# Kernel tuning notes

Measured on AMD Instinct MI355X. Metric: run time of the kernel, lower is better.

The kernel has to match this reference:

```python
import jax, jax.numpy as jnp
import numpy as np

N, K, D, H = 10000, 30, 128, 4
DH = D // H
E = N * K

def setup_inputs() -> dict:
    ks = jax.random.split(jax.random.key(0), 12)
    s = 0.05
    h = jax.random.normal(ks[0], (N, D), jnp.float32)
    e = jax.random.normal(ks[1], (E, D), jnp.float32)
    # edges grouped by source node, K neighbors each (required by the (i j) rearranges)
    src = jnp.repeat(jnp.arange(N, dtype=jnp.int32), K)
    dst = jax.random.randint(ks[2], (E,), 0, N, dtype=jnp.int32)
    edge_index = jnp.stack([src, dst], axis=0)
    return {
        'h': h, 'e': e, 'edge_index': edge_index,
        'att_w1': jax.random.normal(ks[3], (3 * D, D)) * s, 'att_b1': jnp.zeros((D,)),
        'att_w2': jax.random.normal(ks[4], (D, D)) * s,     'att_b2': jnp.zeros((D,)),
        'att_w3': jax.random.normal(ks[5], (D, H)) * s,     'att_b3': jnp.zeros((H,)),
        'node_w1': jax.random.normal(ks[6], (2 * D, D)) * s, 'node_b1': jnp.zeros((D,)),
        'node_w2': jax.random.normal(ks[7], (D, D)) * s,     'node_b2': jnp.zeros((D,)),
        'node_w3': jax.random.normal(ks[8], (D, D)) * s,     'node_b3': jnp.zeros((D,)),
        'to_h_w': jax.random.normal(ks[9], (D, D)) * s,
    }

def reference(h, e, edge_index, att_w1, att_b1, att_w2, att_b2, att_w3, att_b3,
              node_w1, node_b1, node_w2, node_b2, node_w3, node_b3, to_h_w):
    gelu = lambda x: jax.nn.gelu(x, approximate=False)  # torch nn.GELU default (erf)
    hi = h[edge_index[0]]                               # [E, D] gather
    hj = h[edge_index[1]]                               # [E, D] gather
    hi_eij_hj = jnp.concatenate([hi, e, hj], axis=-1)   # [E, 3D]
    eij_hj = jnp.concatenate([e, hj], axis=-1)          # [E, 2D]
    # attention logits per head
    w = jax.nn.relu(hi_eij_hj @ att_w1 + att_b1)
    w = jax.nn.relu(w @ att_w2 + att_b2)
    w = (w @ att_w3 + att_b3).reshape(N, K, H)          # (i j) h -> i j h
    w = w / jnp.sqrt(jnp.float32(DH))
    att = jax.nn.softmax(w, axis=1)                     # softmax over neighbors j
    # values per edge, split per head
    v = gelu(eij_hj @ node_w1 + node_b1)
    v = gelu(v @ node_w2 + node_b2)
    v = (v @ node_w3 + node_b3).reshape(N, K, H, DH)    # (i j) (h d) -> i j h d
    out = jnp.einsum('nkh,nkhd->nhd', att, v).reshape(N, D)  # weighted aggregation
    return out @ to_h_w
```

## Files before the change

kernel.cpp:

```cpp
#include <hip/hip_runtime.h>
#include <hip/hip_bf16.h>

#define N_NODES 10000
#define KNEI    30
#define DIM     128
#define EDGES   (N_NODES * KNEI)

typedef __attribute__((ext_vector_type(4))) float  f32x4;
typedef __attribute__((ext_vector_type(8))) __bf16 bf16x8;
typedef __attribute__((ext_vector_type(4))) __bf16 bf16x4;

#define OFF_AW1 0
#define OFF_AW2 49152
#define OFF_NW1 65536
#define OFF_NW2 98304
#define OFF_NW3 114688
#define OFF_TH  131072
#define TOT_TILES 288
#define YHI_BYTE_OFF (300 * 1024)

__global__ __launch_bounds__(256) void repack_all(
    const float* __restrict__ aw1, const float* __restrict__ aw2,
    const float* __restrict__ nw1, const float* __restrict__ nw2,
    const float* __restrict__ nw3, const float* __restrict__ thw,
    __bf16* __restrict__ dst) {
    int t = blockIdx.x * 256 + threadIdx.x;
    if (t >= TOT_TILES * 512) return;
    int tile = t >> 9;
    const float* src; int lt;
    if      (tile < 96)  { src = aw1; lt = tile; }
    else if (tile < 128) { src = aw2; lt = tile - 96; }
    else if (tile < 192) { src = nw1; lt = tile - 128; }
    else if (tile < 224) { src = nw2; lt = tile - 192; }
    else if (tile < 256) { src = nw3; lt = tile - 224; }
    else                 { src = thw; lt = tile - 256; }
    int i    = t & 7;
    int lane = (t >> 3) & 63;
    int nt = lt & 7;
    int kt = lt >> 3;
    int k = kt * 32 + ((lane >> 4) << 3) + i;
    int n = nt * 16 + (lane & 15);
    dst[t] = (__bf16)src[k * DIM + n];
}

__device__ __forceinline__ float gelu_f(float x) {
    float u = 0.7978845608f * (x + 0.044715f * x * x * x);
    float t = 1.f - 2.f / (__expf(2.f * u) + 1.f);
    return 0.5f * x * (1.f + t);
}

__device__ __forceinline__ bf16x4 cvt4(float4 v) {
    bf16x4 r;
    r[0] = (__bf16)v.x; r[1] = (__bf16)v.y; r[2] = (__bf16)v.z; r[3] = (__bf16)v.w;
    return r;
}

__device__ __forceinline__ void mm_lds4(f32x4 acc[2][2], const __bf16* __restrict__ wfrag,
                                        const __bf16* x, int sx, int nkt,
                                        int wv, int lane) {
    const int mrow = lane & 15;
    const int kgrp = lane >> 4;
#pragma unroll
    for (int kt = 0; kt < nkt; ++kt) {
        bf16x8 a0 = *reinterpret_cast<const bf16x8*>(wfrag + ((kt * 8 + wv * 2 + 0) * 64 + lane) * 8);
        bf16x8 a1 = *reinterpret_cast<const bf16x8*>(wfrag + ((kt * 8 + wv * 2 + 1) * 64 + lane) * 8);
        const int kb = kt * 32 + kgrp * 8;
        bf16x8 b0 = *reinterpret_cast<const bf16x8*>(x + mrow * sx + kb);
        bf16x8 b1 = *reinterpret_cast<const bf16x8*>(x + (16 + mrow) * sx + kb);
        acc[0][0] = __builtin_amdgcn_mfma_f32_16x16x32_bf16(a0, b0, acc[0][0], 0, 0, 0);
        acc[0][1] = __builtin_amdgcn_mfma_f32_16x16x32_bf16(a0, b1, acc[0][1], 0, 0, 0);
        acc[1][0] = __builtin_amdgcn_mfma_f32_16x16x32_bf16(a1, b0, acc[1][0], 0, 0, 0);
        acc[1][1] = __builtin_amdgcn_mfma_f32_16x16x32_bf16(a1, b1, acc[1][1], 0, 0, 0);
    }
}

__device__ __forceinline__ void store_act4(f32x4 acc[2][2], const float* __restrict__ bias,
                                           __bf16* y, int sy, int actmode,
                                           int wv, int lane) {
    const int mrow = lane & 15;
    const int kgrp = lane >> 4;
#pragma unroll
    for (int nt = 0; nt < 2; ++nt) {
        const int nb = wv * 32 + nt * 16 + kgrp * 4;
        float b0 = bias[nb], b1 = bias[nb + 1], b2 = bias[nb + 2], b3 = bias[nb + 3];
#pragma unroll
        for (int mf = 0; mf < 2; ++mf) {
            bf16x4 pk;
            float vv[4] = {acc[nt][mf][0] + b0, acc[nt][mf][1] + b1,
                           acc[nt][mf][2] + b2, acc[nt][mf][3] + b3};
#pragma unroll
            for (int r = 0; r < 4; ++r) {
                float v = vv[r];
                v = actmode == 0 ? fmaxf(v, 0.f) : gelu_f(v);
                pk[r] = (__bf16)v;
            }
            *reinterpret_cast<bf16x4*>(y + (mf * 16 + mrow) * sy + nb) = pk;
        }
    }
}

#define ZERO4(A) do { A[0][0]=(f32x4){0.f,0.f,0.f,0.f}; A[0][1]=(f32x4){0.f,0.f,0.f,0.f}; \
                      A[1][0]=(f32x4){0.f,0.f,0.f,0.f}; A[1][1]=(f32x4){0.f,0.f,0.f,0.f}; } while (0)

__global__ __launch_bounds__(512) void mm128(const float* __restrict__ in,
                                             float* __restrict__ outp,
                                             const __bf16* __restrict__ wfrag,
                                             const float* __restrict__ bias) {
    __shared__ __bf16 sP[64 * 136];
    const int tid  = threadIdx.x;
    const int wv   = tid >> 6;
    const int lane = tid & 63;
    const int mrow = lane & 15;
    const int kgrp = lane >> 4;
    const int base = blockIdx.x * 64;

#pragma unroll
    for (int c = 0; c < 4; ++c) {
        int idx = c * 512 + tid;
        int m  = idx >> 5;
        int jv = idx & 31;
        int row = base + m;
        float4 v = make_float4(0.f, 0.f, 0.f, 0.f);
        if (row < N_NODES) v = *reinterpret_cast<const float4*>(in + (long)row * DIM + jv * 4);
        *reinterpret_cast<bf16x4*>(&sP[m * 136 + jv * 4]) = cvt4(v);
    }
    __syncthreads();

    f32x4 acc[4];
#pragma unroll
    for (int mf = 0; mf < 4; ++mf) acc[mf] = (f32x4){0.f, 0.f, 0.f, 0.f};
#pragma unroll
    for (int kt = 0; kt < 4; ++kt) {
        bf16x8 a = *reinterpret_cast<const bf16x8*>(wfrag + ((kt * 8 + wv) * 64 + lane) * 8);
        const int kb = kt * 32 + kgrp * 8;
#pragma unroll
        for (int mf = 0; mf < 4; ++mf) {
            bf16x8 b = *reinterpret_cast<const bf16x8*>(sP + (mf * 16 + mrow) * 136 + kb);
            acc[mf] = __builtin_amdgcn_mfma_f32_16x16x32_bf16(a, b, acc[mf], 0, 0, 0);
        }
    }
    const int nb = wv * 16 + kgrp * 4;
    float b0 = 0.f, b1 = 0.f, b2 = 0.f, b3 = 0.f;
    if (bias) { b0 = bias[nb]; b1 = bias[nb + 1]; b2 = bias[nb + 2]; b3 = bias[nb + 3]; }
#pragma unroll
    for (int mf = 0; mf < 4; ++mf) {
        int row = base + mf * 16 + mrow;
        if (row < N_NODES) {
            float4 o = make_float4(acc[mf][0] + b0, acc[mf][1] + b1,
                                   acc[mf][2] + b2, acc[mf][3] + b3);
            *reinterpret_cast<float4*>(outp + (long)row * DIM + nb) = o;
        }
    }
}

__global__ __launch_bounds__(256, 4) void gnn_fused(
    const float* __restrict__ h, const float* __restrict__ e, const int* __restrict__ eidx,
    const float* __restrict__ yhi,
    const float* __restrict__ ab2, const float* __restrict__ aw3, const float* __restrict__ ab3,
    const float* __restrict__ nb1, const float* __restrict__ nb2, const float* __restrict__ nb3,
    const __bf16* __restrict__ wp, float* __restrict__ pre_out) {

    __shared__ __bf16 S[32 * 264];
    __shared__ __bf16 Y1[32 * 136];
    __shared__ __bf16 Y2[32 * 136];
    __shared__ float  sLogW[4][32][4];
    __shared__ float  sW[32][4];

    const int tid  = threadIdx.x;
    const int wv   = tid >> 6;
    const int lane = tid & 63;
    const int mrow = lane & 15;
    const int kg   = lane >> 4;
    const int node = blockIdx.x;
    const long ebase = (long)node * KNEI;

#pragma unroll
    for (int c = 0; c < 4; ++c) {
        int idx = c * 256 + tid;
        int m  = idx >> 5;
        int jv = idx & 31;
        float4 ev = make_float4(0.f, 0.f, 0.f, 0.f), hjv = ev;
        if (m < KNEI) {
            long ge = ebase + m;
            ev  = *reinterpret_cast<const float4*>(e + ge * DIM + jv * 4);
            int dstn = eidx[EDGES + ge];
            hjv = *reinterpret_cast<const float4*>(h + (long)dstn * DIM + jv * 4);
        }
        *reinterpret_cast<bf16x4*>(&S[m * 264 + jv * 4])       = cvt4(ev);
        *reinterpret_cast<bf16x4*>(&S[m * 264 + 128 + jv * 4]) = cvt4(hjv);
    }
    __syncthreads();

    f32x4 acc[2][2];

    ZERO4(acc);
    mm_lds4(acc, wp + OFF_AW1 + 16384, S, 264, 8, wv, lane);
    store_act4(acc, yhi + (long)node * DIM, Y1, 136, 0, wv, lane);
    __syncthreads();

    {
        ZERO4(acc);
        mm_lds4(acc, wp + OFF_AW2, Y1, 136, 4, wv, lane);
        float lp[2][4];
        lp[0][0]=lp[0][1]=lp[0][2]=lp[0][3]=0.f;
        lp[1][0]=lp[1][1]=lp[1][2]=lp[1][3]=0.f;
#pragma unroll
        for (int nt = 0; nt < 2; ++nt) {
            const int nb = wv * 32 + nt * 16 + kg * 4;
            float b0 = ab2[nb], b1 = ab2[nb + 1], b2 = ab2[nb + 2], b3 = ab2[nb + 3];
            float4 w3v[4];
#pragma unroll
            for (int r = 0; r < 4; ++r)
                w3v[r] = *reinterpret_cast<const float4*>(aw3 + (nb + r) * 4);
#pragma unroll
            for (int mf = 0; mf < 2; ++mf) {
                float vv[4] = {acc[nt][mf][0] + b0, acc[nt][mf][1] + b1,
                               acc[nt][mf][2] + b2, acc[nt][mf][3] + b3};
#pragma unroll
                for (int r = 0; r < 4; ++r) {
                    float v = fmaxf(vv[r], 0.f);
                    lp[mf][0] += v * w3v[r].x;
                    lp[mf][1] += v * w3v[r].y;
                    lp[mf][2] += v * w3v[r].z;
                    lp[mf][3] += v * w3v[r].w;
                }
            }
        }
#pragma unroll
        for (int mf = 0; mf < 2; ++mf)
#pragma unroll
            for (int hh = 0; hh < 4; ++hh) {
                lp[mf][hh] += __shfl_xor(lp[mf][hh], 16);
                lp[mf][hh] += __shfl_xor(lp[mf][hh], 32);
            }
        if (kg == 0) {
#pragma unroll
            for (int mf = 0; mf < 2; ++mf) {
                float4 o = make_float4(lp[mf][0], lp[mf][1], lp[mf][2], lp[mf][3]);
                *reinterpret_cast<float4*>(&sLogW[wv][mf * 16 + mrow][0]) = o;
            }
        }
    }
    ZERO4(acc);
    mm_lds4(acc, wp + OFF_NW1, S, 264, 8, wv, lane);
    store_act4(acc, nb1, Y2, 136, 1, wv, lane);
    __syncthreads();

    if (tid < 128) {
        int m = tid >> 2, hh = tid & 3;
        float s = ab3[hh];
#pragma unroll
        for (int w = 0; w < 4; ++w) s += sLogW[w][m][hh];
        sLogW[0][m][hh] = s * 0.17677669529f;
    }
    ZERO4(acc);
    mm_lds4(acc, wp + OFF_NW2, Y2, 136, 4, wv, lane);
    store_act4(acc, nb2, Y1, 136, 1, wv, lane);
    __syncthreads();

    if (wv == 0 && lane < 32) {
        float4 lg = (lane < KNEI) ? *reinterpret_cast<float4*>(&sLogW[0][lane][0])
                                  : make_float4(-1e30f, -1e30f, -1e30f, -1e30f);
        float4 mx = lg;
#pragma unroll
        for (int msk = 1; msk <= 16; msk <<= 1) {
            mx.x = fmaxf(mx.x, __shfl_xor(mx.x, msk));
            mx.y = fmaxf(mx.y, __shfl_xor(mx.y, msk));
            mx.z = fmaxf(mx.z, __shfl_xor(mx.z, msk));
            mx.w = fmaxf(mx.w, __shfl_xor(mx.w, msk));
        }
        float4 ex = make_float4(__expf(lg.x - mx.x), __expf(lg.y - mx.y),
                                __expf(lg.z - mx.z), __expf(lg.w - mx.w));
        float4 sm = ex;
#pragma unroll
        for (int msk = 1; msk <= 16; msk <<= 1) {
            sm.x += __shfl_xor(sm.x, msk);
            sm.y += __shfl_xor(sm.y, msk);
            sm.z += __shfl_xor(sm.z, msk);
            sm.w += __shfl_xor(sm.w, msk);
        }
        float4 w = make_float4(ex.x / sm.x, ex.y / sm.y, ex.z / sm.z, ex.w / sm.w);
        *reinterpret_cast<float4*>(&sW[lane][0]) = w;
    }
    ZERO4(acc);
    mm_lds4(acc, wp + OFF_NW3, Y1, 136, 4, wv, lane);
    __syncthreads();

    {
        float wgt0 = sW[mrow][wv];
        float wgt1 = sW[16 + mrow][wv];
        float part[2][4];
#pragma unroll
        for (int nt = 0; nt < 2; ++nt)
#pragma unroll
            for (int r = 0; r < 4; ++r)
                part[nt][r] = wgt0 * acc[nt][0][r] + wgt1 * acc[nt][1][r];
#pragma unroll
        for (int msk = 1; msk <= 8; msk <<= 1)
#pragma unroll
            for (int nt = 0; nt < 2; ++nt)
#pragma unroll
                for (int r = 0; r < 4; ++r)
                    part[nt][r] += __shfl_xor(part[nt][r], msk);
        if (mrow == 0) {
#pragma unroll
            for (int nt = 0; nt < 2; ++nt) {
                const int nb = wv * 32 + nt * 16 + kg * 4;
                float4 o = make_float4(part[nt][0] + nb3[nb],     part[nt][1] + nb3[nb + 1],
                                       part[nt][2] + nb3[nb + 2], part[nt][3] + nb3[nb + 3]);
                *reinterpret_cast<float4*>(pre_out + (long)node * DIM + nb) = o;
            }
        }
    }
}

extern "C" void kernel_launch(void* const* d_in, const int* in_sizes, int n_in,
                              void* d_out, int out_size, void* d_ws, size_t ws_size,
                              hipStream_t stream) {
    const float* h   = (const float*)d_in[0];
    const float* e   = (const float*)d_in[1];
    const int*   ei  = (const int*)d_in[2];
    const float* aw1 = (const float*)d_in[3];
    const float* ab1 = (const float*)d_in[4];
    const float* aw2 = (const float*)d_in[5];
    const float* ab2 = (const float*)d_in[6];
    const float* aw3 = (const float*)d_in[7];
    const float* ab3 = (const float*)d_in[8];
    const float* nw1 = (const float*)d_in[9];
    const float* nb1 = (const float*)d_in[10];
    const float* nw2 = (const float*)d_in[11];
    const float* nb2 = (const float*)d_in[12];
    const float* nw3 = (const float*)d_in[13];
    const float* nb3 = (const float*)d_in[14];
    const float* thw = (const float*)d_in[15];
    float* out = (float*)d_out;
    __bf16* wp = (__bf16*)d_ws;
    float* yhi = (float*)((char*)d_ws + YHI_BYTE_OFF);

    repack_all<<<TOT_TILES * 2, 256, 0, stream>>>(aw1, aw2, nw1, nw2, nw3, thw, wp);

    const int nblk = (N_NODES + 63) / 64;
    mm128<<<nblk, 512, 0, stream>>>(h, yhi, wp + OFF_AW1, ab1);

    gnn_fused<<<N_NODES, 256, 0, stream>>>(h, e, ei, yhi, ab2, aw3, ab3,
                                           nb1, nb2, nb3, wp, out);
    mm128<<<nblk, 512, 0, stream>>>(out, out, wp + OFF_TH, nullptr);
}
```

Before: 179.7 us.

## Merge attention and value MLP layers into wide concatenated GEMMs with shared LDS

Repacks weights so the first layers of the attention and value MLPs form one 256-wide GEMM over the shared [e,hj] tile, and the second layers form one block-diagonal-style pass where waves 0-1 handle attention and waves 2-3 handle values. This reuses each B fragment across four MFMAs and cuts the number of separate matmul phases and barriers. LDS is collapsed into one reused buffer and the occupancy hint is raised from 4 to 6 blocks. The cost is more accumulator registers per wave (acc[4][2]) and uneven epilogue work between attention and value waves.

```diff
diff --git a/kernel.cpp b/kernel.cpp
--- a/kernel.cpp
+++ b/kernel.cpp
@@ -10,11 +10,10 @@
 typedef __attribute__((ext_vector_type(8))) __bf16 bf16x8;
 typedef __attribute__((ext_vector_type(4))) __bf16 bf16x4;
 
-#define OFF_AW1 0
-#define OFF_AW2 49152
-#define OFF_NW1 65536
-#define OFF_NW2 98304
-#define OFF_NW3 114688
+#define OFF_CW1 0
+#define OFF_CW2 65536
+#define OFF_NW3 98304
+#define OFF_HI  114688
 #define OFF_TH  131072
 #define TOT_TILES 288
 #define YHI_BYTE_OFF (300 * 1024)
@@ -27,20 +26,28 @@
     int t = blockIdx.x * 256 + threadIdx.x;
     if (t >= TOT_TILES * 512) return;
     int tile = t >> 9;
-    const float* src; int lt;
-    if      (tile < 96)  { src = aw1; lt = tile; }
-    else if (tile < 128) { src = aw2; lt = tile - 96; }
-    else if (tile < 192) { src = nw1; lt = tile - 128; }
-    else if (tile < 224) { src = nw2; lt = tile - 192; }
-    else if (tile < 256) { src = nw3; lt = tile - 224; }
-    else                 { src = thw; lt = tile - 256; }
     int i    = t & 7;
     int lane = (t >> 3) & 63;
-    int nt = lt & 7;
-    int kt = lt >> 3;
-    int k = kt * 32 + ((lane >> 4) << 3) + i;
-    int n = nt * 16 + (lane & 15);
-    dst[t] = (__bf16)src[k * DIM + n];
+    int krow = ((lane >> 4) << 3) + i;
+    int ncol = lane & 15;
+    float v;
+    if (tile < 128) {
+        int kt = tile >> 4, nt = tile & 15;
+        int k = kt * 32 + krow, n = nt * 16 + ncol;
+        v = (n < 128) ? aw1[(128 + k) * 128 + n] : nw1[k * 128 + (n - 128)];
+    } else if (tile < 192) {
+        int lt = tile - 128;
+        int kt = lt >> 4, nt = lt & 15;
+        int k = kt * 32 + krow, n = nt * 16 + ncol;
+        v = (n < 128) ? aw2[k * 128 + n] : nw2[k * 128 + (n - 128)];
+    } else {
+        int lt = tile & 31;
+        int kt = lt >> 3, nt = lt & 7;
+        int k = kt * 32 + krow, n = nt * 16 + ncol;
+        const float* s = (tile < 224) ? nw3 : (tile < 256) ? aw1 : thw;
+        v = s[k * 128 + n];
+    }
+    dst[t] = (__bf16)v;
 }
 
 __device__ __forceinline__ float gelu_f(float x) {
@@ -54,53 +61,6 @@
     r[0] = (__bf16)v.x; r[1] = (__bf16)v.y; r[2] = (__bf16)v.z; r[3] = (__bf16)v.w;
     return r;
 }
-
-__device__ __forceinline__ void mm_lds4(f32x4 acc[2][2], const __bf16* __restrict__ wfrag,
-                                        const __bf16* x, int sx, int nkt,
-                                        int wv, int lane) {
-    const int mrow = lane & 15;
-    const int kgrp = lane >> 4;
-#pragma unroll
-    for (int kt = 0; kt < nkt; ++kt) {
-        bf16x8 a0 = *reinterpret_cast<const bf16x8*>(wfrag + ((kt * 8 + wv * 2 + 0) * 64 + lane) * 8);
-        bf16x8 a1 = *reinterpret_cast<const bf16x8*>(wfrag + ((kt * 8 + wv * 2 + 1) * 64 + lane) * 8);
-        const int kb = kt * 32 + kgrp * 8;
-        bf16x8 b0 = *reinterpret_cast<const bf16x8*>(x + mrow * sx + kb);
-        bf16x8 b1 = *reinterpret_cast<const bf16x8*>(x + (16 + mrow) * sx + kb);
-        acc[0][0] = __builtin_amdgcn_mfma_f32_16x16x32_bf16(a0, b0, acc[0][0], 0, 0, 0);
-        acc[0][1] = __builtin_amdgcn_mfma_f32_16x16x32_bf16(a0, b1, acc[0][1], 0, 0, 0);
-        acc[1][0] = __builtin_amdgcn_mfma_f32_16x16x32_bf16(a1, b0, acc[1][0], 0, 0, 0);
-        acc[1][1] = __builtin_amdgcn_mfma_f32_16x16x32_bf16(a1, b1, acc[1][1], 0, 0, 0);
-    }
-}
-
-__device__ __forceinline__ void store_act4(f32x4 acc[2][2], const float* __restrict__ bias,
-                                           __bf16* y, int sy, int actmode,
-                                           int wv, int lane) {
-    const int mrow = lane & 15;
-    const int kgrp = lane >> 4;
-#pragma unroll
-    for (int nt = 0; nt < 2; ++nt) {
-        const int nb = wv * 32 + nt * 16 + kgrp * 4;
-        float b0 = bias[nb], b1 = bias[nb + 1], b2 = bias[nb + 2], b3 = bias[nb + 3];
-#pragma unroll
-        for (int mf = 0; mf < 2; ++mf) {
-            bf16x4 pk;
-            float vv[4] = {acc[nt][mf][0] + b0, acc[nt][mf][1] + b1,
-                           acc[nt][mf][2] + b2, acc[nt][mf][3] + b3};
-#pragma unroll
-            for (int r = 0; r < 4; ++r) {
-                float v = vv[r];
-                v = actmode == 0 ? fmaxf(v, 0.f) : gelu_f(v);
-                pk[r] = (__bf16)v;
-            }
-            *reinterpret_cast<bf16x4*>(y + (mf * 16 + mrow) * sy + nb) = pk;
-        }
-    }
-}
-
-#define ZERO4(A) do { A[0][0]=(f32x4){0.f,0.f,0.f,0.f}; A[0][1]=(f32x4){0.f,0.f,0.f,0.f}; \
-                      A[1][0]=(f32x4){0.f,0.f,0.f,0.f}; A[1][1]=(f32x4){0.f,0.f,0.f,0.f}; } while (0)
 
 __global__ __launch_bounds__(512) void mm128(const float* __restrict__ in,
                                              float* __restrict__ outp,
@@ -153,17 +113,15 @@
     }
 }
 
-__global__ __launch_bounds__(256, 4) void gnn_fused(
+__global__ __launch_bounds__(256, 6) void gnn_fused(
     const float* __restrict__ h, const float* __restrict__ e, const int* __restrict__ eidx,
     const float* __restrict__ yhi,
     const float* __restrict__ ab2, const float* __restrict__ aw3, const float* __restrict__ ab3,
     const float* __restrict__ nb1, const float* __restrict__ nb2, const float* __restrict__ nb3,
     const __bf16* __restrict__ wp, float* __restrict__ pre_out) {
 
-    __shared__ __bf16 S[32 * 264];
-    __shared__ __bf16 Y1[32 * 136];
-    __shared__ __bf16 Y2[32 * 136];
-    __shared__ float  sLogW[4][32][4];
+    __shared__ __bf16 U[8704];
+    __shared__ float  sLP[2][32][4];
     __shared__ float  sW[32][4];
 
     const int tid  = threadIdx.x;
@@ -186,36 +144,95 @@
             int dstn = eidx[EDGES + ge];
             hjv = *reinterpret_cast<const float4*>(h + (long)dstn * DIM + jv * 4);
         }
-        *reinterpret_cast<bf16x4*>(&S[m * 264 + jv * 4])       = cvt4(ev);
-        *reinterpret_cast<bf16x4*>(&S[m * 264 + 128 + jv * 4]) = cvt4(hjv);
-    }
-    __syncthreads();
-
-    f32x4 acc[2][2];
-
-    ZERO4(acc);
-    mm_lds4(acc, wp + OFF_AW1 + 16384, S, 264, 8, wv, lane);
-    store_act4(acc, yhi + (long)node * DIM, Y1, 136, 0, wv, lane);
-    __syncthreads();
-
-    {
-        ZERO4(acc);
-        mm_lds4(acc, wp + OFF_AW2, Y1, 136, 4, wv, lane);
+        *reinterpret_cast<bf16x4*>(&U[m * 264 + jv * 4])       = cvt4(ev);
+        *reinterpret_cast<bf16x4*>(&U[m * 264 + 128 + jv * 4]) = cvt4(hjv);
+    }
+    __syncthreads();
+
+    f32x4 acc[4][2];
+#pragma unroll
+    for (int j = 0; j < 4; ++j) { acc[j][0] = (f32x4){0.f,0.f,0.f,0.f}; acc[j][1] = (f32x4){0.f,0.f,0.f,0.f}; }
+
+    {
+        const __bf16* b0p = U + mrow * 264;
+        const __bf16* b1p = U + (16 + mrow) * 264;
+#pragma unroll
+        for (int kt = 0; kt < 8; ++kt) {
+            const int kb = kt * 32 + kg * 8;
+            bf16x8 b0 = *reinterpret_cast<const bf16x8*>(b0p + kb);
+            bf16x8 b1 = *reinterpret_cast<const bf16x8*>(b1p + kb);
+#pragma unroll
+            for (int j = 0; j < 4; ++j) {
+                bf16x8 a = *reinterpret_cast<const bf16x8*>(wp + OFF_CW1 + (size_t)((kt * 16 + wv * 4 + j) * 64 + lane) * 8);
+                acc[j][0] = __builtin_amdgcn_mfma_f32_16x16x32_bf16(a, b0, acc[j][0], 0, 0, 0);
+                acc[j][1] = __builtin_amdgcn_mfma_f32_16x16x32_bf16(a, b1, acc[j][1], 0, 0, 0);
+            }
+        }
+    }
+    __syncthreads();
+
+    {
+        const bool isatt = (wv < 2);
+        __bf16* Y = U + (isatt ? 0 : 4352);
+        const float* yrow = yhi + (long)node * DIM;
+#pragma unroll
+        for (int j = 0; j < 4; ++j) {
+            const int f = (wv & 1) * 64 + j * 16 + kg * 4;
+            float b0, b1, b2, b3;
+            if (isatt) { b0 = yrow[f]; b1 = yrow[f+1]; b2 = yrow[f+2]; b3 = yrow[f+3]; }
+            else       { b0 = nb1[f];  b1 = nb1[f+1];  b2 = nb1[f+2];  b3 = nb1[f+3]; }
+#pragma unroll
+            for (int mf = 0; mf < 2; ++mf) {
+                float vv[4] = {acc[j][mf][0] + b0, acc[j][mf][1] + b1,
+                               acc[j][mf][2] + b2, acc[j][mf][3] + b3};
+                bf16x4 pk;
+#pragma unroll
+                for (int r = 0; r < 4; ++r) {
+                    float v = isatt ? fmaxf(vv[r], 0.f) : gelu_f(vv[r]);
+                    pk[r] = (__bf16)v;
+                }
+                *reinterpret_cast<bf16x4*>(Y + (mf * 16 + mrow) * 136 + f) = pk;
+            }
+        }
+    }
+    __syncthreads();
+
+#pragma unroll
+    for (int j = 0; j < 4; ++j) { acc[j][0] = (f32x4){0.f,0.f,0.f,0.f}; acc[j][1] = (f32x4){0.f,0.f,0.f,0.f}; }
+    {
+        const __bf16* Yb = U + ((wv < 2) ? 0 : 4352);
+        const __bf16* b0p = Yb + mrow * 136;
+        const __bf16* b1p = Yb + (16 + mrow) * 136;
+#pragma unroll
+        for (int kt = 0; kt < 4; ++kt) {
+            const int kb = kt * 32 + kg * 8;
+            bf16x8 b0 = *reinterpret_cast<const bf16x8*>(b0p + kb);
+            bf16x8 b1 = *reinterpret_cast<const bf16x8*>(b1p + kb);
+#pragma unroll
+            for (int j = 0; j < 4; ++j) {
+                bf16x8 a = *reinterpret_cast<const bf16x8*>(wp + OFF_CW2 + (size_t)((kt * 16 + wv * 4 + j) * 64 + lane) * 8);
+                acc[j][0] = __builtin_amdgcn_mfma_f32_16x16x32_bf16(a, b0, acc[j][0], 0, 0, 0);
+                acc[j][1] = __builtin_amdgcn_mfma_f32_16x16x32_bf16(a, b1, acc[j][1], 0, 0, 0);
+            }
+        }
+    }
+
+    if (wv < 2) {
         float lp[2][4];
         lp[0][0]=lp[0][1]=lp[0][2]=lp[0][3]=0.f;
         lp[1][0]=lp[1][1]=lp[1][2]=lp[1][3]=0.f;
 #pragma unroll
-        for (int nt = 0; nt < 2; ++nt) {
-            const int nb = wv * 32 + nt * 16 + kg * 4;
-            float b0 = ab2[nb], b1 = ab2[nb + 1], b2 = ab2[nb + 2], b3 = ab2[nb + 3];
+        for (int j = 0; j < 4; ++j) {
+            const int f = (wv & 1) * 64 + j * 16 + kg * 4;
+            float b0 = ab2[f], b1 = ab2[f+1], b2 = ab2[f+2], b3 = ab2[f+3];
             float4 w3v[4];
 #pragma unroll
             for (int r = 0; r < 4; ++r)
-                w3v[r] = *reinterpret_cast<const float4*>(aw3 + (nb + r) * 4);
+                w3v[r] = *reinterpret_cast<const float4*>(aw3 + (f + r) * 4);
 #pragma unroll
             for (int mf = 0; mf < 2; ++mf) {
-                float vv[4] = {acc[nt][mf][0] + b0, acc[nt][mf][1] + b1,
-                               acc[nt][mf][2] + b2, acc[nt][mf][3] + b3};
+                float vv[4] = {acc[j][mf][0] + b0, acc[j][mf][1] + b1,
+                               acc[j][mf][2] + b2, acc[j][mf][3] + b3};
 #pragma unroll
                 for (int r = 0; r < 4; ++r) {
                     float v = fmaxf(vv[r], 0.f);
@@ -237,30 +254,58 @@
 #pragma unroll
             for (int mf = 0; mf < 2; ++mf) {
                 float4 o = make_float4(lp[mf][0], lp[mf][1], lp[mf][2], lp[mf][3]);
-                *reinterpret_cast<float4*>(&sLogW[wv][mf * 16 + mrow][0]) = o;
-            }
-        }
-    }
-    ZERO4(acc);
-    mm_lds4(acc, wp + OFF_NW1, S, 264, 8, wv, lane);
-    store_act4(acc, nb1, Y2, 136, 1, wv, lane);
-    __syncthreads();
-
-    if (tid < 128) {
-        int m = tid >> 2, hh = tid & 3;
-        float s = ab3[hh];
-#pragma unroll
-        for (int w = 0; w < 4; ++w) s += sLogW[w][m][hh];
-        sLogW[0][m][hh] = s * 0.17677669529f;
-    }
-    ZERO4(acc);
-    mm_lds4(acc, wp + OFF_NW2, Y2, 136, 4, wv, lane);
-    store_act4(acc, nb2, Y1, 136, 1, wv, lane);
-    __syncthreads();
-
+                *reinterpret_cast<float4*>(&sLP[wv][mf * 16 + mrow][0]) = o;
+            }
+        }
+    }
+    __syncthreads();
+
+    if (wv >= 2) {
+#pragma unroll
+        for (int j = 0; j < 4; ++j) {
+            const int f = (wv & 1) * 64 + j * 16 + kg * 4;
+            float b0 = nb2[f], b1 = nb2[f+1], b2 = nb2[f+2], b3 = nb2[f+3];
+#pragma unroll
+            for (int mf = 0; mf < 2; ++mf) {
+                float vv[4] = {acc[j][mf][0] + b0, acc[j][mf][1] + b1,
+                               acc[j][mf][2] + b2, acc[j][mf][3] + b3};
+                bf16x4 pk;
+#pragma unroll
+                for (int r = 0; r < 4; ++r) pk[r] = (__bf16)gelu_f(vv[r]);
+                *reinterpret_cast<bf16x4*>(U + (mf * 16 + mrow) * 136 + f) = pk;
+            }
+        }
+    }
+    __syncthreads();
+
+    f32x4 a2[2][2];
+    a2[0][0]=(f32x4){0.f,0.f,0.f,0.f}; a2[0][1]=(f32x4){0.f,0.f,0.f,0.f};
+    a2[1][0]=(f32x4){0.f,0.f,0.f,0.f}; a2[1][1]=(f32x4){0.f,0.f,0.f,0.f};
+    {
+        const __bf16* b0p = U + mrow * 136;
+        const __bf16* b1p = U + (16 + mrow) * 136;
+#pragma unroll
+        for (int kt = 0; kt < 4; ++kt) {
+            const int kb = kt * 32 + kg * 8;
+            bf16x8 b0 = *reinterpret_cast<const bf16x8*>(b0p + kb);
+            bf16x8 b1 = *reinterpret_cast<const bf16x8*>(b1p + kb);
+#pragma unroll
+            for (int j = 0; j < 2; ++j) {
+                bf16x8 a = *reinterpret_cast<const bf16x8*>(wp + OFF_NW3 + (size_t)((kt * 8 + wv * 2 + j) * 64 + lane) * 8);
+                a2[j][0] = __builtin_amdgcn_mfma_f32_16x16x32_bf16(a, b0, a2[j][0], 0, 0, 0);
+                a2[j][1] = __builtin_amdgcn_mfma_f32_16x16x32_bf16(a, b1, a2[j][1], 0, 0, 0);
+            }
+        }
+    }
     if (wv == 0 && lane < 32) {
-        float4 lg = (lane < KNEI) ? *reinterpret_cast<float4*>(&sLogW[0][lane][0])
-                                  : make_float4(-1e30f, -1e30f, -1e30f, -1e30f);
+        const float s = 0.17677669529f;
+        float4 lg;
+        if (lane < KNEI) {
+            float4 p0 = *reinterpret_cast<float4*>(&sLP[0][lane][0]);
+            float4 p1 = *reinterpret_cast<float4*>(&sLP[1][lane][0]);
+            lg = make_float4((p0.x + p1.x + ab3[0]) * s, (p0.y + p1.y + ab3[1]) * s,
+                             (p0.z + p1.z + ab3[2]) * s, (p0.w + p1.w + ab3[3]) * s);
+        } else lg = make_float4(-1e30f, -1e30f, -1e30f, -1e30f);
         float4 mx = lg;
 #pragma unroll
         for (int msk = 1; msk <= 16; msk <<= 1) {
@@ -282,8 +327,6 @@
         float4 w = make_float4(ex.x / sm.x, ex.y / sm.y, ex.z / sm.z, ex.w / sm.w);
         *reinterpret_cast<float4*>(&sW[lane][0]) = w;
     }
-    ZERO4(acc);
-    mm_lds4(acc, wp + OFF_NW3, Y1, 136, 4, wv, lane);
     __syncthreads();
 
     {
@@ -291,23 +334,23 @@
         float wgt1 = sW[16 + mrow][wv];
         float part[2][4];
 #pragma unroll
-        for (int nt = 0; nt < 2; ++nt)
+        for (int j = 0; j < 2; ++j)
 #pragma unroll
             for (int r = 0; r < 4; ++r)
-                part[nt][r] = wgt0 * acc[nt][0][r] + wgt1 * acc[nt][1][r];
+                part[j][r] = wgt0 * a2[j][0][r] + wgt1 * a2[j][1][r];
 #pragma unroll
         for (int msk = 1; msk <= 8; msk <<= 1)
 #pragma unroll
-            for (int nt = 0; nt < 2; ++nt)
+            for (int j = 0; j < 2; ++j)
 #pragma unroll
                 for (int r = 0; r < 4; ++r)
-                    part[nt][r] += __shfl_xor(part[nt][r], msk);
+                    part[j][r] += __shfl_xor(part[j][r], msk);
         if (mrow == 0) {
 #pragma unroll
-            for (int nt = 0; nt < 2; ++nt) {
-                const int nb = wv * 32 + nt * 16 + kg * 4;
-                float4 o = make_float4(part[nt][0] + nb3[nb],     part[nt][1] + nb3[nb + 1],
-                                       part[nt][2] + nb3[nb + 2], part[nt][3] + nb3[nb + 3]);
+            for (int j = 0; j < 2; ++j) {
+                const int nb = wv * 32 + j * 16 + kg * 4;
+                float4 o = make_float4(part[j][0] + nb3[nb],     part[j][1] + nb3[nb + 1],
+                                       part[j][2] + nb3[nb + 2], part[j][3] + nb3[nb + 3]);
                 *reinterpret_cast<float4*>(pre_out + (long)node * DIM + nb) = o;
             }
         }
@@ -340,7 +383,7 @@
     repack_all<<<TOT_TILES * 2, 256, 0, stream>>>(aw1, aw2, nw1, nw2, nw3, thw, wp);
 
     const int nblk = (N_NODES + 63) / 64;
-    mm128<<<nblk, 512, 0, stream>>>(h, yhi, wp + OFF_AW1, ab1);
+    mm128<<<nblk, 512, 0, stream>>>(h, yhi, wp + OFF_HI, ab1);
 
     gnn_fused<<<N_NODES, 256, 0, stream>>>(h, e, ei, yhi, ab2, aw3, ab3,
                                            nb1, nb2, nb3, wp, out);
```

After: 211.4 us. 17.7% more time.

## Use 8 waves per node block, each owning one 16-column MFMA tile

Applied to the files above, without the earlier changes.

The fused per-node kernel now launches 512 threads (8 waves) instead of 256. Each wave computes a single 16-wide output column tile rather than two, so accumulators shrink from 2x2 to 2 per wave and the logit partial buffer doubles to 8 slots. The NW3 matmul is also moved ahead of the softmax so it can overlap with wave 0's reduction. More waves per block adds latency hiding, but each wave reloads the B fragments from LDS, so LDS traffic doubles and per-CU occupancy may drop under the launch bound.

```diff
diff --git a/kernel.cpp b/kernel.cpp
--- a/kernel.cpp
+++ b/kernel.cpp
@@ -27,6 +27,8 @@
     int t = blockIdx.x * 256 + threadIdx.x;
     if (t >= TOT_TILES * 512) return;
     int tile = t >> 9;
+    int i    = t & 7;
+    int lane = (t >> 3) & 63;
     const float* src; int lt;
     if      (tile < 96)  { src = aw1; lt = tile; }
     else if (tile < 128) { src = aw2; lt = tile - 96; }
@@ -34,8 +36,6 @@
     else if (tile < 224) { src = nw2; lt = tile - 192; }
     else if (tile < 256) { src = nw3; lt = tile - 224; }
     else                 { src = thw; lt = tile - 256; }
-    int i    = t & 7;
-    int lane = (t >> 3) & 63;
     int nt = lt & 7;
     int kt = lt >> 3;
     int k = kt * 32 + ((lane >> 4) << 3) + i;
@@ -55,52 +55,45 @@
     return r;
 }
 
-__device__ __forceinline__ void mm_lds4(f32x4 acc[2][2], const __bf16* __restrict__ wfrag,
-                                        const __bf16* x, int sx, int nkt,
-                                        int wv, int lane) {
+__device__ __forceinline__ void mm_lds(f32x4 acc[2], const __bf16* __restrict__ wfrag,
+                                       const __bf16* x, int sx, int nkt,
+                                       int wv, int lane) {
     const int mrow = lane & 15;
-    const int kgrp = lane >> 4;
+    const int kgrp = (lane >> 4) & 3;
 #pragma unroll
     for (int kt = 0; kt < nkt; ++kt) {
-        bf16x8 a0 = *reinterpret_cast<const bf16x8*>(wfrag + ((kt * 8 + wv * 2 + 0) * 64 + lane) * 8);
-        bf16x8 a1 = *reinterpret_cast<const bf16x8*>(wfrag + ((kt * 8 + wv * 2 + 1) * 64 + lane) * 8);
+        bf16x8 a = *reinterpret_cast<const bf16x8*>(wfrag + ((kt * 8 + wv) * 64 + lane) * 8);
         const int kb = kt * 32 + kgrp * 8;
-        bf16x8 b0 = *reinterpret_cast<const bf16x8*>(x + mrow * sx + kb);
-        bf16x8 b1 = *reinterpret_cast<const bf16x8*>(x + (16 + mrow) * sx + kb);
-        acc[0][0] = __builtin_amdgcn_mfma_f32_16x16x32_bf16(a0, b0, acc[0][0], 0, 0, 0);
-        acc[0][1] = __builtin_amdgcn_mfma_f32_16x16x32_bf16(a0, b1, acc[0][1], 0, 0, 0);
-        acc[1][0] = __builtin_amdgcn_mfma_f32_16x16x32_bf16(a1, b0, acc[1][0], 0, 0, 0);
-        acc[1][1] = __builtin_amdgcn_mfma_f32_16x16x32_bf16(a1, b1, acc[1][1], 0, 0, 0);
-    }
-}
-
-__device__ __forceinline__ void store_act4(f32x4 acc[2][2], const float* __restrict__ bias,
-                                           __bf16* y, int sy, int actmode,
-                                           int wv, int lane) {
+#pragma unroll
+        for (int mf = 0; mf < 2; ++mf) {
+            bf16x8 b = *reinterpret_cast<const bf16x8*>(x + (mf * 16 + mrow) * sx + kb);
+            acc[mf] = __builtin_amdgcn_mfma_f32_16x16x32_bf16(a, b, acc[mf], 0, 0, 0);
+        }
+    }
+}
+
+__device__ __forceinline__ void store_act(f32x4 acc[2], const float* __restrict__ bias,
+                                          __bf16* y, int sy, int actmode,
+                                          int wv, int lane) {
     const int mrow = lane & 15;
-    const int kgrp = lane >> 4;
-#pragma unroll
-    for (int nt = 0; nt < 2; ++nt) {
-        const int nb = wv * 32 + nt * 16 + kgrp * 4;
-        float b0 = bias[nb], b1 = bias[nb + 1], b2 = bias[nb + 2], b3 = bias[nb + 3];
-#pragma unroll
-        for (int mf = 0; mf < 2; ++mf) {
-            bf16x4 pk;
-            float vv[4] = {acc[nt][mf][0] + b0, acc[nt][mf][1] + b1,
-                           acc[nt][mf][2] + b2, acc[nt][mf][3] + b3};
-#pragma unroll
-            for (int r = 0; r < 4; ++r) {
-                float v = vv[r];
-                v = actmode == 0 ? fmaxf(v, 0.f) : gelu_f(v);
-                pk[r] = (__bf16)v;
-            }
-            *reinterpret_cast<bf16x4*>(y + (mf * 16 + mrow) * sy + nb) = pk;
-        }
-    }
-}
-
-#define ZERO4(A) do { A[0][0]=(f32x4){0.f,0.f,0.f,0.f}; A[0][1]=(f32x4){0.f,0.f,0.f,0.f}; \
-                      A[1][0]=(f32x4){0.f,0.f,0.f,0.f}; A[1][1]=(f32x4){0.f,0.f,0.f,0.f}; } while (0)
+    const int kgrp = (lane >> 4) & 3;
+    const int nb = wv * 16 + kgrp * 4;
+    float b0 = bias[nb], b1 = bias[nb + 1], b2 = bias[nb + 2], b3 = bias[nb + 3];
+#pragma unroll
+    for (int mf = 0; mf < 2; ++mf) {
+        bf16x4 pk;
+        float vv[4] = {acc[mf][0] + b0, acc[mf][1] + b1, acc[mf][2] + b2, acc[mf][3] + b3};
+#pragma unroll
+        for (int r = 0; r < 4; ++r) {
+            float v = vv[r];
+            v = actmode == 0 ? fmaxf(v, 0.f) : gelu_f(v);
+            pk[r] = (__bf16)v;
+        }
+        *reinterpret_cast<bf16x4*>(y + (mf * 16 + mrow) * sy + nb) = pk;
+    }
+}
+
+#define ZERO2(A) do { A[0] = (f32x4){0.f,0.f,0.f,0.f}; A[1] = (f32x4){0.f,0.f,0.f,0.f}; } while (0)
 
 __global__ __launch_bounds__(512) void mm128(const float* __restrict__ in,
                                              float* __restrict__ outp,
@@ -153,7 +146,7 @@
     }
 }
 
-__global__ __launch_bounds__(256, 4) void gnn_fused(
+__global__ __launch_bounds__(512, 4) void gnn_fused(
     const float* __restrict__ h, const float* __restrict__ e, const int* __restrict__ eidx,
     const float* __restrict__ yhi,
     const float* __restrict__ ab2, const float* __restrict__ aw3, const float* __restrict__ ab3,
@@ -163,20 +156,20 @@
     __shared__ __bf16 S[32 * 264];
     __shared__ __bf16 Y1[32 * 136];
     __shared__ __bf16 Y2[32 * 136];
-    __shared__ float  sLogW[4][32][4];
+    __shared__ float  sLogW[8][32][4];
     __shared__ float  sW[32][4];
 
     const int tid  = threadIdx.x;
     const int wv   = tid >> 6;
     const int lane = tid & 63;
     const int mrow = lane & 15;
-    const int kg   = lane >> 4;
+    const int kg   = (lane >> 4) & 3;
     const int node = blockIdx.x;
     const long ebase = (long)node * KNEI;
 
 #pragma unroll
-    for (int c = 0; c < 4; ++c) {
-        int idx = c * 256 + tid;
+    for (int c = 0; c < 2; ++c) {
+        int idx = c * 512 + tid;
         int m  = idx >> 5;
         int jv = idx & 31;
         float4 ev = make_float4(0.f, 0.f, 0.f, 0.f), hjv = ev;
@@ -191,39 +184,34 @@
     }
     __syncthreads();
 
-    f32x4 acc[2][2];
-
-    ZERO4(acc);
-    mm_lds4(acc, wp + OFF_AW1 + 16384, S, 264, 8, wv, lane);
-    store_act4(acc, yhi + (long)node * DIM, Y1, 136, 0, wv, lane);
+    f32x4 acc[2];
+
+    ZERO2(acc);
+    mm_lds(acc, wp + OFF_AW1 + 16384, S, 264, 8, wv, lane);
+    store_act(acc, yhi + (long)node * DIM, Y1, 136, 0, wv, lane);
     __syncthreads();
 
     {
-        ZERO4(acc);
-        mm_lds4(acc, wp + OFF_AW2, Y1, 136, 4, wv, lane);
+        ZERO2(acc);
+        mm_lds(acc, wp + OFF_AW2, Y1, 136, 4, wv, lane);
+        const int nb = wv * 16 + kg * 4;
+        float b0 = ab2[nb], b1 = ab2[nb + 1], b2 = ab2[nb + 2], b3 = ab2[nb + 3];
+        float4 w3v[4];
+#pragma unroll
+        for (int r = 0; r < 4; ++r)
+            w3v[r] = *reinterpret_cast<const float4*>(aw3 + (nb + r) * 4);
         float lp[2][4];
-        lp[0][0]=lp[0][1]=lp[0][2]=lp[0][3]=0.f;
-        lp[1][0]=lp[1][1]=lp[1][2]=lp[1][3]=0.f;
-#pragma unroll
-        for (int nt = 0; nt < 2; ++nt) {
-            const int nb = wv * 32 + nt * 16 + kg * 4;
-            float b0 = ab2[nb], b1 = ab2[nb + 1], b2 = ab2[nb + 2], b3 = ab2[nb + 3];
-            float4 w3v[4];
-#pragma unroll
-            for (int r = 0; r < 4; ++r)
-                w3v[r] = *reinterpret_cast<const float4*>(aw3 + (nb + r) * 4);
-#pragma unroll
-            for (int mf = 0; mf < 2; ++mf) {
-                float vv[4] = {acc[nt][mf][0] + b0, acc[nt][mf][1] + b1,
-                               acc[nt][mf][2] + b2, acc[nt][mf][3] + b3};
-#pragma unroll
-                for (int r = 0; r < 4; ++r) {
-                    float v = fmaxf(vv[r], 0.f);
-                    lp[mf][0] += v * w3v[r].x;
-                    lp[mf][1] += v * w3v[r].y;
-                    lp[mf][2] += v * w3v[r].z;
-                    lp[mf][3] += v * w3v[r].w;
-                }
+#pragma unroll
+        for (int mf = 0; mf < 2; ++mf) {
+            lp[mf][0] = lp[mf][1] = lp[mf][2] = lp[mf][3] = 0.f;
+            float vv[4] = {acc[mf][0] + b0, acc[mf][1] + b1, acc[mf][2] + b2, acc[mf][3] + b3};
+#pragma unroll
+            for (int r = 0; r < 4; ++r) {
+                float v = fmaxf(vv[r], 0.f);
+                lp[mf][0] += v * w3v[r].x;
+                lp[mf][1] += v * w3v[r].y;
+                lp[mf][2] += v * w3v[r].z;
+                lp[mf][3] += v * w3v[r].w;
             }
         }
 #pragma unroll
@@ -233,7 +221,7 @@
                 lp[mf][hh] += __shfl_xor(lp[mf][hh], 16);
                 lp[mf][hh] += __shfl_xor(lp[mf][hh], 32);
             }
-        if (kg == 0) {
+        if (kg == 0 && lane < 16) {
 #pragma unroll
             for (int mf = 0; mf < 2; ++mf) {
                 float4 o = make_float4(lp[mf][0], lp[mf][1], lp[mf][2], lp[mf][3]);
@@ -241,23 +229,25 @@
             }
         }
     }
-    ZERO4(acc);
-    mm_lds4(acc, wp + OFF_NW1, S, 264, 8, wv, lane);
-    store_act4(acc, nb1, Y2, 136, 1, wv, lane);
+    ZERO2(acc);
+    mm_lds(acc, wp + OFF_NW1, S, 264, 8, wv, lane);
+    store_act(acc, nb1, Y2, 136, 1, wv, lane);
     __syncthreads();
 
     if (tid < 128) {
         int m = tid >> 2, hh = tid & 3;
         float s = ab3[hh];
 #pragma unroll
-        for (int w = 0; w < 4; ++w) s += sLogW[w][m][hh];
+        for (int w = 0; w < 8; ++w) s += sLogW[w][m][hh];
         sLogW[0][m][hh] = s * 0.17677669529f;
     }
-    ZERO4(acc);
-    mm_lds4(acc, wp + OFF_NW2, Y2, 136, 4, wv, lane);
-    store_act4(acc, nb2, Y1, 136, 1, wv, lane);
-    __syncthreads();
-
+    ZERO2(acc);
+    mm_lds(acc, wp + OFF_NW2, Y2, 136, 4, wv, lane);
+    store_act(acc, nb2, Y1, 136, 1, wv, lane);
+    __syncthreads();
+
+    ZERO2(acc);
+    mm_lds(acc, wp + OFF_NW3, Y1, 136, 4, wv, lane);
     if (wv == 0 && lane < 32) {
         float4 lg = (lane < KNEI) ? *reinterpret_cast<float4*>(&sLogW[0][lane][0])
                                   : make_float4(-1e30f, -1e30f, -1e30f, -1e30f);
@@ -282,34 +272,26 @@
         float4 w = make_float4(ex.x / sm.x, ex.y / sm.y, ex.z / sm.z, ex.w / sm.w);
         *reinterpret_cast<float4*>(&sW[lane][0]) = w;
     }
-    ZERO4(acc);
-    mm_lds4(acc, wp + OFF_NW3, Y1, 136, 4, wv, lane);
     __syncthreads();
 
     {
-        float wgt0 = sW[mrow][wv];
-        float wgt1 = sW[16 + mrow][wv];
-        float part[2][4];
-#pragma unroll
-        for (int nt = 0; nt < 2; ++nt)
+        const int hh = wv >> 1;
+        float wgt0 = sW[mrow][hh];
+        float wgt1 = sW[16 + mrow][hh];
+        float part[4];
+#pragma unroll
+        for (int r = 0; r < 4; ++r)
+            part[r] = wgt0 * acc[0][r] + wgt1 * acc[1][r];
+#pragma unroll
+        for (int msk = 1; msk <= 8; msk <<= 1)
 #pragma unroll
             for (int r = 0; r < 4; ++r)
-                part[nt][r] = wgt0 * acc[nt][0][r] + wgt1 * acc[nt][1][r];
-#pragma unroll
-        for (int msk = 1; msk <= 8; msk <<= 1)
-#pragma unroll
-            for (int nt = 0; nt < 2; ++nt)
-#pragma unroll
-                for (int r = 0; r < 4; ++r)
-                    part[nt][r] += __shfl_xor(part[nt][r], msk);
+                part[r] += __shfl_xor(part[r], msk);
         if (mrow == 0) {
-#pragma unroll
-            for (int nt = 0; nt < 2; ++nt) {
-                const int nb = wv * 32 + nt * 16 + kg * 4;
-                float4 o = make_float4(part[nt][0] + nb3[nb],     part[nt][1] + nb3[nb + 1],
-                                       part[nt][2] + nb3[nb + 2], part[nt][3] + nb3[nb + 3]);
-                *reinterpret_cast<float4*>(pre_out + (long)node * DIM + nb) = o;
-            }
+            const int nb = wv * 16 + kg * 4;
+            float4 o = make_float4(part[0] + nb3[nb],     part[1] + nb3[nb + 1],
+                                   part[2] + nb3[nb + 2], part[3] + nb3[nb + 3]);
+            *reinterpret_cast<float4*>(pre_out + (long)node * DIM + nb) = o;
         }
     }
 }
@@ -342,7 +324,7 @@
     const int nblk = (N_NODES + 63) / 64;
     mm128<<<nblk, 512, 0, stream>>>(h, yhi, wp + OFF_AW1, ab1);
 
-    gnn_fused<<<N_NODES, 256, 0, stream>>>(h, e, ei, yhi, ab2, aw3, ab3,
+    gnn_fused<<<N_NODES, 512, 0, stream>>>(h, e, ei, yhi, ab2, aw3, ab3,
                                            nb1, nb2, nb3, wp, out);
     mm128<<<nblk, 512, 0, stream>>>(out, out, wp + OFF_TH, nullptr);
 }
```

After: 179.6 us. No clear change (-0.0%).
